# Kernel tuning notes

Measured on AMD Instinct MI355X. Metric: run time of the kernel, lower is better.

Reference implementation:

```python
import jax, jax.numpy as jnp
import numpy as np

NPOINT = 1024
NSAMPLE = 32
RADIUS = 0.2


def index_points2(points, idx):
    # points: (B,N,D), idx: (B,S) -> (B,S,D)
    return jnp.take_along_axis(points, idx[..., None], axis=1)


def index_points3(points, idx):
    # points: (B,N,D), idx: (B,S,K) -> (B,S,K,D)
    B, S, K = idx.shape
    flat = jnp.take_along_axis(points, idx.reshape(B, S * K)[..., None], axis=1)
    return flat.reshape(B, S, K, points.shape[-1])


def farthest_point_sampling(xyz, npoint):
    # xyz: (B,N,3) -> (B,npoint) int32 indices. First point deterministic (index 0).
    B, N, _ = xyz.shape
    first = jnp.zeros((B,), jnp.int32)
    chosen = jnp.zeros((B, npoint), jnp.int32).at[:, 0].set(first)
    first_xyz = index_points2(xyz, first[:, None])[:, 0, :]
    dist_min = jnp.sum((xyz - first_xyz[:, None, :]) ** 2, axis=-1)  # (B,N)

    def body(i, carry):
        chosen, dist_min = carry
        far = jnp.argmax(dist_min, axis=-1).astype(jnp.int32)  # (B,)
        far_xyz = index_points2(xyz, far[:, None])[:, 0, :]
        d = jnp.sum((xyz - far_xyz[:, None, :]) ** 2, axis=-1)
        return chosen.at[:, i].set(far), jnp.minimum(dist_min, d)

    chosen, _ = jax.lax.fori_loop(1, npoint, body, (chosen, dist_min))
    return chosen


def query_ball_point(radius, nsample, xyz, new_xyz):
    # (B,S,N) squared distances; out-of-ball -> inf; take nsample nearest (stable argsort).
    dist = jnp.sum((new_xyz[:, :, None, :] - xyz[:, None, :, :]) ** 2, axis=-1)
    dist_m = jnp.where(dist <= radius ** 2, dist, jnp.inf)
    return jnp.argsort(dist_m, axis=-1)[:, :, :nsample]


def mlp2(x, Wa, ba, Wb, bb, act2):
    h = jax.nn.relu(x @ Wa + ba)
    return act2(h @ Wb + bb)


def reference(xyz, features, W1, b1, W2, b2, W3, b3, W4, b4):
    fps_idx = farthest_point_sampling(xyz, NPOINT)          # (B,S)
    new_xyz = index_points2(xyz, fps_idx)                   # (B,S,3)
    group_idx = query_ball_point(RADIUS, NSAMPLE, xyz, new_xyz)  # (B,S,K)
    grouped_xyz = index_points3(xyz, group_idx)             # (B,S,K,3)
    grouped_xyz_norm = grouped_xyz - new_xyz[:, :, None, :]
    grouped_feats = index_points3(features, group_idx)      # (B,S,K,C)
    f_in = jnp.concatenate([grouped_xyz_norm, grouped_feats], axis=-1)
    f_prime = mlp2(f_in, W1, b1, W2, b2, jax.nn.relu)       # (B,S,K,H)
    f_mean = jnp.mean(f_prime, axis=2, keepdims=True)
    w_in = jnp.concatenate([grouped_xyz_norm, f_prime - f_mean], axis=-1)
    alpha = mlp2(w_in, W3, b3, W4, b4, jax.nn.sigmoid)      # (B,S,K,H)
    f_out = jnp.sum(alpha * f_prime, axis=2)                # (B,S,H)
    return new_xyz, f_out


def setup_inputs() -> dict:
    key = jax.random.key(0)
    ks = jax.random.split(key, 8)
    B, N, C, H = 16, 4096, 64, 128
    xyz = jax.random.uniform(ks[0], (B, N, 3), dtype=jnp.float32)
    features = jax.random.normal(ks[1], (B, N, C), dtype=jnp.float32)
    s = 0.1
    return {
        "xyz": xyz,
        "features": features,
        "W1": jax.random.normal(ks[2], (3 + C, H), dtype=jnp.float32) * s,
        "b1": jnp.zeros((H,), jnp.float32),
        "W2": jax.random.normal(ks[3], (H, H), dtype=jnp.float32) * s,
        "b2": jnp.zeros((H,), jnp.float32),
        "W3": jax.random.normal(ks[4], (3 + H, H), dtype=jnp.float32) * s,
        "b3": jnp.zeros((H,), jnp.float32),
        "W4": jax.random.normal(ks[5], (H, H), dtype=jnp.float32) * s,
        "b4": jnp.zeros((H,), jnp.float32),
    }
```

## Files before the change

kernel.cpp:

```cpp
#include <hip/hip_runtime.h>

typedef unsigned short u16;
typedef unsigned int   u32;
typedef unsigned long long u64;
typedef short s8v __attribute__((ext_vector_type(8)));
typedef float f4v __attribute__((ext_vector_type(4)));
typedef float f2v __attribute__((ext_vector_type(2)));

#define STRIDE 168
#define CAP 256
#define OFF_G1 0
#define OFF_G2 12288
#define OFF_G3 28672
#define OFF_G4 49152

__device__ __forceinline__ float bf2f(u16 u){ return __uint_as_float(((u32)u)<<16); }
__device__ __forceinline__ u16 f2bf(float f){
  u32 u = __float_as_uint(f);
  return (u16)((u + 0x7FFFu + ((u>>16)&1u)) >> 16);
}
__device__ __forceinline__ float sqd(float ax,float ay,float az,float bx,float by,float bz){
  float dx=ax-bx, dy=ay-by, dz=az-bz;
  return __fadd_rn(__fadd_rn(__fmul_rn(dx,dx),__fmul_rn(dy,dy)),__fmul_rn(dz,dz));
}

#define WMAX_STEP(v, CTRL) { \
  u32 _t = (u32)__builtin_amdgcn_update_dpp(0, (int)(v), CTRL, 0xf, 0xf, false); \
  (v) = (v) > _t ? (v) : _t; }
#define QMAX64(k, CTRL) { \
  u32 _lo=(u32)(k), _hi=(u32)((k)>>32); \
  u32 _plo=(u32)__builtin_amdgcn_update_dpp(0,(int)_lo,CTRL,0xf,0xf,true); \
  u32 _phi=(u32)__builtin_amdgcn_update_dpp(0,(int)_hi,CTRL,0xf,0xf,true); \
  u64 _o=((u64)_phi<<32)|_plo; (k) = (k)>_o ? (k) : _o; }

__global__ __launch_bounds__(256) void fps_kernel(const float* __restrict__ xyz,
                                                  float* __restrict__ newxyz){
  __shared__ __align__(16) float S[4096*3];
  __shared__ __align__(16) float R[1024*3];
  __shared__ u64 red[2][4];
  const int b = blockIdx.x, tid = threadIdx.x;
  const int lane = tid & 63, wv = tid >> 6;
  const float* xb = xyz + (size_t)b*4096*3;
  #pragma unroll
  for(int j=0;j<12;j++) ((float4*)S)[j*256+tid] = ((const float4*)xb)[j*256+tid];
  __syncthreads();
  f2v X[8],Y[8],Z[8],DM[8];
  const float x0=S[0], y0=S[1], z0=S[2];
  {
    #pragma clang fp contract(off)
    const f2v fx2={x0,x0}, fy2={y0,y0}, fz2={z0,z0};
    #pragma unroll
    for(int k2=0;k2<8;k2++){
      int p0 = tid*16 + 2*k2;
      X[k2] = (f2v){S[p0*3],   S[p0*3+3]};
      Y[k2] = (f2v){S[p0*3+1], S[p0*3+4]};
      Z[k2] = (f2v){S[p0*3+2], S[p0*3+5]};
      f2v dx=X[k2]-fx2, dy=Y[k2]-fy2, dz=Z[k2]-fz2;
      DM[k2] = (dx*dx + dy*dy) + dz*dz;
    }
  }
  if(tid==0){ R[0]=x0; R[1]=y0; R[2]=z0; }
  for(int i=1;i<1024;i++){
    f2v a = __builtin_elementwise_max(__builtin_elementwise_max(DM[0],DM[1]),
                                      __builtin_elementwise_max(DM[2],DM[3]));
    f2v c = __builtin_elementwise_max(__builtin_elementwise_max(DM[4],DM[5]),
                                      __builtin_elementwise_max(DM[6],DM[7]));
    f2v mm = __builtin_elementwise_max(a,c);
    float vm = fmaxf(mm[0], mm[1]);
    u32 m16 = 0;
    #pragma unroll
    for(int j=0;j<16;j++) m16 |= (DM[j>>1][j&1]==vm) ? (1u<<j) : 0u;
    int jm = __ffs(m16)-1;
    u32 w = __float_as_uint(vm);
    WMAX_STEP(w, 0x111); WMAX_STEP(w, 0x112); WMAX_STEP(w, 0x114);
    WMAX_STEP(w, 0x118); WMAX_STEP(w, 0x142); WMAX_STEP(w, 0x143);
    u32 wm = (u32)__builtin_amdgcn_readlane((int)w, 63);
    u64 msk = __ballot(__float_as_uint(vm) == wm);
    int ldr = __ffsll((unsigned long long)msk) - 1;
    int pj  = __builtin_amdgcn_readlane(jm, ldr);
    int p   = (wv*64 + ldr)*16 + pj;
    if(lane==0) red[i&1][wv] = ((u64)wm<<32) | (u32)(~(u32)p);
    __syncthreads();
    u64 k = red[i&1][lane&3];
    QMAX64(k, 0xB1); QMAX64(k, 0x4E);
    int far = (int)(~(u32)k) & 4095;
    float fx=S[far*3], fy=S[far*3+1], fz=S[far*3+2];
    if(tid==0){ R[i*3]=fx; R[i*3+1]=fy; R[i*3+2]=fz; }
    {
      #pragma clang fp contract(off)
      const f2v fx2={fx,fx}, fy2={fy,fy}, fz2={fz,fz};
      #pragma unroll
      for(int k2c=0;k2c<8;k2c++){
        f2v dx=X[k2c]-fx2, dy=Y[k2c]-fy2, dz=Z[k2c]-fz2;
        f2v s = (dx*dx + dy*dy) + dz*dz;
        DM[k2c] = __builtin_elementwise_min(DM[k2c], s);
      }
    }
  }
  __syncthreads();
  float* nb = newxyz + (size_t)b*3072;
  #pragma unroll
  for(int j=0;j<3;j++) ((float4*)nb)[j*256+tid] = ((const float4*)R)[j*256+tid];
}

__global__ __launch_bounds__(256) void swz_kernel(const float* __restrict__ W1,const float* __restrict__ W2,
                                                  const float* __restrict__ W3,const float* __restrict__ W4,
                                                  u16* __restrict__ wsw){
  int T = blockIdx.x*256 + threadIdx.x;
  const float* W; int rel, base, kind;
  if(T < 1536){ rel=T;      base=OFF_G1; W=W1; kind=0; }
  else if(T < 3584){ rel=T-1536; base=OFF_G2; W=W2; kind=1; }
  else if(T < 6144){ rel=T-3584; base=OFF_G3; W=W3; kind=0; }
  else         { rel=T-6144; base=OFF_G4; W=W4; kind=1; }
  int chunk=rel>>6, lane=rel&63, c=chunk>>3, t=chunk&7, quad=lane>>4, l15=lane&15;
  u16 v[8];
  #pragma unroll
  for(int j=0;j<8;j++){
    int kp = c*32 + quad*8 + j, n = t*16 + l15;
    int src = (kind==0) ? (kp<3 ? kp : (kp>=32 ? kp-29 : -1)) : kp;
    v[j] = (src<0) ? (u16)0 : f2bf(W[src*128 + n]);
  }
  int4 o;
  o.x=(int)((u32)v[0]|((u32)v[1]<<16)); o.y=(int)((u32)v[2]|((u32)v[3]<<16));
  o.z=(int)((u32)v[4]|((u32)v[5]<<16)); o.w=(int)((u32)v[6]|((u32)v[7]<<16));
  *(int4*)&wsw[base + rel*8] = o;
}

__device__ __forceinline__ void zero_C(f4v C[2][8]){
  #pragma unroll
  for(int mt=0;mt<2;mt++)
    #pragma unroll
    for(int t=0;t<8;t++) C[mt][t] = (f4v){0.f,0.f,0.f,0.f};
}
__device__ __forceinline__ void load_bias(const float* bsrc,int l15,float bb[8]){
  #pragma unroll
  for(int t=0;t<8;t++) bb[t]=bsrc[t*16+l15];
}
template<int KC>
__device__ __forceinline__ void run_gemm(const u16* A, const u16* BW,
                                         int lane,int l15,int quad, f4v C[2][8]){
  s8v af[2][KC];
  #pragma unroll
  for(int mt=0;mt<2;mt++)
    #pragma unroll
    for(int c=0;c<KC;c++)
      af[mt][c] = *(const s8v*)&A[(mt*16+l15)*STRIDE + c*32 + quad*8];
  #pragma unroll
  for(int t=0;t<8;t++){
    #pragma unroll
    for(int c=0;c<KC;c++){
      s8v bw = *(const s8v*)&BW[((c*8+t)*64 + lane)*8];
      C[0][t] = __builtin_amdgcn_mfma_f32_16x16x32_bf16(af[0][c],bw,C[0][t],0,0,0);
      C[1][t] = __builtin_amdgcn_mfma_f32_16x16x32_bf16(af[1][c],bw,C[1][t],0,0,0);
    }
  }
}
__device__ __forceinline__ void store_act(u16* A,int l15,int quad,f4v C[2][8],const float bb[8]){
  #pragma unroll
  for(int mt=0;mt<2;mt++)
    #pragma unroll
    for(int t=0;t<8;t++)
      #pragma unroll
      for(int r=0;r<4;r++){
        float v = fmaxf(C[mt][t][r]+bb[t], 0.f);
        A[(mt*16+quad*4+r)*STRIDE + t*16 + l15] = f2bf(v);
      }
}
__device__ __forceinline__ void write_xyz_chunk0(u16* A,int lane,float xn,float yn,float zn){
  if(lane<32){
    u16* row=&A[lane*STRIDE];
    row[0]=f2bf(xn); row[1]=f2bf(yn); row[2]=f2bf(zn); row[3]=0;
    #pragma unroll
    for(int q=0;q<7;q++) *(u64*)&row[4+q*4] = 0ull;
  }
}

__global__ __launch_bounds__(256,3) void mlp_kernel(const float* __restrict__ xyz,
    const float* __restrict__ feats, const u16* __restrict__ wsw,
    const float* __restrict__ b1,const float* __restrict__ b2,const float* __restrict__ b3,const float* __restrict__ b4,
    const float* __restrict__ newxyz, float* __restrict__ fout){
  __shared__ __align__(16) u16 Abuf[4][32*STRIDE];
  __shared__ u64 Bcand[4][CAP];
  __shared__ int selbuf[4][32];
  const int tid=threadIdx.x, wv=tid>>6, lane=tid&63, quad=lane>>4, l15=lane&15;
  const int widx = blockIdx.x*4 + wv, b = widx>>10;
  u16* A = Abuf[wv];
  const float* xb = xyz + (size_t)b*4096*3;
  const float cx=newxyz[widx*3], cy=newxyz[widx*3+1], cz=newxyz[widx*3+2];

  {
    u64* Bc = Bcand[wv];
    int* sel = selbuf[wv];
    const u64 lt = (1ull<<lane)-1ull;
    int base=0;
    for(int kk=0;kk<64;kk++){
      int p = kk*64 + lane;
      float d = sqd(cx,cy,cz, xb[p*3],xb[p*3+1],xb[p*3+2]);
      bool in = (d <= 0.04f);
      u64 m = __ballot(in);
      if(in){ int pos = base + __popcll(m&lt); if(pos<CAP) Bc[pos] = ((u64)__float_as_uint(d)<<32)|(u32)p; }
      base += __popcll(m);
    }
    int cnt = base>CAP ? CAP : base;
    if(cnt > 32){
      for(int c=lane; c<cnt; c+=64){
        u64 key = Bc[c]; int r=0;
        for(int t2=0;t2<cnt;t2++) r += (Bc[t2] < key) ? 1 : 0;
        if(r < 32) sel[r] = (int)(u32)key;
      }
    } else {
      for(int c=lane; c<cnt; c+=64) sel[c] = (int)(u32)Bc[c];
      int need = 32 - cnt, b2 = 0;
      for(int kk=0; kk<64 && b2<need; kk++){
        int p = kk*64 + lane;
        float d = sqd(cx,cy,cz, xb[p*3],xb[p*3+1],xb[p*3+2]);
        bool o = !(d <= 0.04f);
        u64 m = __ballot(o);
        if(o){ int pos = b2 + __popcll(m&lt); if(pos<need) sel[cnt+pos] = p; }
        b2 += __popcll(m);
      }
    }
  }
  const int* sel = selbuf[wv];
  const int gi_f = sel[lane>>1] & 4095;
  const int gi_x = sel[lane & 31] & 4095;

  {
    int r2=lane>>1, h=lane&1;
    const float* fs = feats + ((size_t)b*4096 + gi_f)*64 + h*32;
    u16* fd = &A[r2*STRIDE + 32 + h*32];
    #pragma unroll
    for(int j=0;j<8;j++){
      float4 v4 = ((const float4*)fs)[j];
      u64 pk4 = (u64)f2bf(v4.x) | ((u64)f2bf(v4.y)<<16)
              | ((u64)f2bf(v4.z)<<32) | ((u64)f2bf(v4.w)<<48);
      *(u64*)&fd[j*4] = pk4;
    }
  }
  float xn=0.f,yn=0.f,zn=0.f;
  if(lane<32){
    const float* xp = xb + (size_t)gi_x*3;
    xn = xp[0]-cx; yn = xp[1]-cy; zn = xp[2]-cz;
  }
  write_xyz_chunk0(A,lane,xn,yn,zn);
  __syncthreads();

  f4v C[2][8]; float bb[8];
  zero_C(C); load_bias(b1,l15,bb);
  run_gemm<3>(A, wsw+OFF_G1, lane,l15,quad, C);
  store_act(A,l15,quad,C,bb);
  __syncthreads();
  zero_C(C); load_bias(b2,l15,bb);
  run_gemm<4>(A, wsw+OFF_G2, lane,l15,quad, C);
  float fp[2][8][4]; float mean[8];
  #pragma unroll
  for(int t=0;t<8;t++){
    float s=0.f;
    #pragma unroll
    for(int mt=0;mt<2;mt++)
      #pragma unroll
      for(int r=0;r<4;r++){
        float v = fmaxf(C[mt][t][r]+bb[t], 0.f);
        fp[mt][t][r]=v; s+=v;
      }
    s += __shfl_xor(s,16); s += __shfl_xor(s,32);
    mean[t] = s*0.03125f;
  }
  #pragma unroll
  for(int mt=0;mt<2;mt++)
    #pragma unroll
    for(int t=0;t<8;t++)
      #pragma unroll
      for(int r=0;r<4;r++)
        A[(mt*16+quad*4+r)*STRIDE + 32 + t*16 + l15] = f2bf(fp[mt][t][r]-mean[t]);
  write_xyz_chunk0(A,lane,xn,yn,zn);
  __syncthreads();
  zero_C(C); load_bias(b3,l15,bb);
  run_gemm<5>(A, wsw+OFF_G3, lane,l15,quad, C);
  store_act(A,l15,quad,C,bb);
  __syncthreads();
  zero_C(C); load_bias(b4,l15,bb);
  run_gemm<4>(A, wsw+OFF_G4, lane,l15,quad, C);
  float* fo = fout + (size_t)widx*128;
  #pragma unroll
  for(int t=0;t<8;t++){
    float part=0.f;
    #pragma unroll
    for(int mt=0;mt<2;mt++)
      #pragma unroll
      for(int r=0;r<4;r++){
        float pre = C[mt][t][r]+bb[t];
        float a = 1.f/(1.f+__expf(-pre));
        part += a*fp[mt][t][r];
      }
    part += __shfl_xor(part,16); part += __shfl_xor(part,32);
    if(quad==0) fo[t*16+l15] = part;
  }
}

extern "C" void kernel_launch(void* const* d_in, const int* in_sizes, int n_in,
                              void* d_out, int out_size, void* d_ws, size_t ws_size,
                              hipStream_t stream){
  (void)in_sizes; (void)n_in; (void)out_size; (void)ws_size;
  const float* xyz   = (const float*)d_in[0];
  const float* feats = (const float*)d_in[1];
  const float* W1 = (const float*)d_in[2]; const float* b1 = (const float*)d_in[3];
  const float* W2 = (const float*)d_in[4]; const float* b2 = (const float*)d_in[5];
  const float* W3 = (const float*)d_in[6]; const float* b3 = (const float*)d_in[7];
  const float* W4 = (const float*)d_in[8]; const float* b4 = (const float*)d_in[9];
  float* out = (float*)d_out;
  float* newxyz = out;
  float* fout   = out + 16*1024*3;
  u16* wsw = (u16*)d_ws;

  hipLaunchKernelGGL(swz_kernel, dim3(32),   dim3(256), 0, stream, W1,W2,W3,W4, wsw);
  hipLaunchKernelGGL(fps_kernel, dim3(16),   dim3(256), 0, stream, xyz, newxyz);
  hipLaunchKernelGGL(mlp_kernel, dim3(4096), dim3(256), 0, stream,
                     xyz, feats, wsw, b1,b2,b3,b4, newxyz, fout);
}
```

Measured before the change: 1.010 ms.

## Run FPS in a single wave and split ball query into its own kernel

FPS now runs one 64-lane wave per batch with 64 points per lane held in registers. It uses a tree argmax with indices, so the cross-wave LDS reduction and the __syncthreads in each of the 1023 iterations go away. Ball query moves out of the MLP kernel into a separate kernel that writes the selected indices into the fout buffer as scratch, and its rank-sort reads two keys at a time. The MLP kernel then only reads those indices, which frees its LDS and may raise occupancy. The cost is an extra launch, a global round-trip for the indices, and much higher register pressure in FPS, which runs on only 16 waves.

```diff
diff --git a/kernel.cpp b/kernel.cpp
--- a/kernel.cpp
+++ b/kernel.cpp
@@ -6,6 +6,8 @@
 typedef short s8v __attribute__((ext_vector_type(8)));
 typedef float f4v __attribute__((ext_vector_type(4)));
 typedef float f2v __attribute__((ext_vector_type(2)));
+typedef int   i2v __attribute__((ext_vector_type(2)));
+typedef unsigned long long ull2 __attribute__((ext_vector_type(2)));
 
 #define STRIDE 168
 #define CAP 256
@@ -27,50 +29,46 @@
 #define WMAX_STEP(v, CTRL) { \
   u32 _t = (u32)__builtin_amdgcn_update_dpp(0, (int)(v), CTRL, 0xf, 0xf, false); \
   (v) = (v) > _t ? (v) : _t; }
-#define QMAX64(k, CTRL) { \
-  u32 _lo=(u32)(k), _hi=(u32)((k)>>32); \
-  u32 _plo=(u32)__builtin_amdgcn_update_dpp(0,(int)_lo,CTRL,0xf,0xf,true); \
-  u32 _phi=(u32)__builtin_amdgcn_update_dpp(0,(int)_hi,CTRL,0xf,0xf,true); \
-  u64 _o=((u64)_phi<<32)|_plo; (k) = (k)>_o ? (k) : _o; }
-
-__global__ __launch_bounds__(256) void fps_kernel(const float* __restrict__ xyz,
-                                                  float* __restrict__ newxyz){
-  __shared__ __align__(16) float S[4096*3];
+
+__global__ __launch_bounds__(64,1) void fps_kernel(const float* __restrict__ xyz,
+                                                   float* __restrict__ newxyz){
+  __shared__ __align__(16) float SX[64][66], SY[64][66], SZ[64][66];
   __shared__ __align__(16) float R[1024*3];
-  __shared__ u64 red[2][4];
-  const int b = blockIdx.x, tid = threadIdx.x;
-  const int lane = tid & 63, wv = tid >> 6;
+  const int b = blockIdx.x, lane = threadIdx.x;
   const float* xb = xyz + (size_t)b*4096*3;
-  #pragma unroll
-  for(int j=0;j<12;j++) ((float4*)S)[j*256+tid] = ((const float4*)xb)[j*256+tid];
-  __syncthreads();
-  f2v X[8],Y[8],Z[8],DM[8];
-  const float x0=S[0], y0=S[1], z0=S[2];
+  for(int j=0;j<64;j++){
+    int p = j*64 + lane;
+    SX[j][lane] = xb[p*3]; SY[j][lane] = xb[p*3+1]; SZ[j][lane] = xb[p*3+2];
+  }
+  f2v X[32],Y[32],Z[32],DM[32];
+  const float x0=SX[0][0], y0=SY[0][0], z0=SZ[0][0];
   {
     #pragma clang fp contract(off)
     const f2v fx2={x0,x0}, fy2={y0,y0}, fz2={z0,z0};
     #pragma unroll
-    for(int k2=0;k2<8;k2++){
-      int p0 = tid*16 + 2*k2;
-      X[k2] = (f2v){S[p0*3],   S[p0*3+3]};
-      Y[k2] = (f2v){S[p0*3+1], S[p0*3+4]};
-      Z[k2] = (f2v){S[p0*3+2], S[p0*3+5]};
-      f2v dx=X[k2]-fx2, dy=Y[k2]-fy2, dz=Z[k2]-fz2;
-      DM[k2] = (dx*dx + dy*dy) + dz*dz;
-    }
-  }
-  if(tid==0){ R[0]=x0; R[1]=y0; R[2]=z0; }
+    for(int k=0;k<32;k++){
+      X[k] = (f2v){SX[lane][k], SX[lane][k+32]};
+      Y[k] = (f2v){SY[lane][k], SY[lane][k+32]};
+      Z[k] = (f2v){SZ[lane][k], SZ[lane][k+32]};
+      f2v dx=X[k]-fx2, dy=Y[k]-fy2, dz=Z[k]-fz2;
+      DM[k] = (dx*dx + dy*dy) + dz*dz;
+    }
+  }
+  if(lane==0){ R[0]=x0; R[1]=y0; R[2]=z0; }
   for(int i=1;i<1024;i++){
-    f2v a = __builtin_elementwise_max(__builtin_elementwise_max(DM[0],DM[1]),
-                                      __builtin_elementwise_max(DM[2],DM[3]));
-    f2v c = __builtin_elementwise_max(__builtin_elementwise_max(DM[4],DM[5]),
-                                      __builtin_elementwise_max(DM[6],DM[7]));
-    f2v mm = __builtin_elementwise_max(a,c);
-    float vm = fmaxf(mm[0], mm[1]);
-    u32 m16 = 0;
-    #pragma unroll
-    for(int j=0;j<16;j++) m16 |= (DM[j>>1][j&1]==vm) ? (1u<<j) : 0u;
-    int jm = __ffs(m16)-1;
+    f2v v[32]; i2v ix[32];
+    #pragma unroll
+    for(int k=0;k<32;k++){ v[k]=DM[k]; ix[k]=(i2v){k, k+32}; }
+    #pragma unroll
+    for(int n=32;n>1;n>>=1)
+      #pragma unroll
+      for(int k=0;k<(n>>1);k++){
+        i2v c = v[2*k+1] > v[2*k];
+        v[k]  = c ? v[2*k+1] : v[2*k];
+        ix[k] = c ? ix[2*k+1] : ix[2*k];
+      }
+    float vm; int jm;
+    { bool g = v[0][1] > v[0][0]; vm = g ? v[0][1] : v[0][0]; jm = g ? ix[0][1] : ix[0][0]; }
     u32 w = __float_as_uint(vm);
     WMAX_STEP(w, 0x111); WMAX_STEP(w, 0x112); WMAX_STEP(w, 0x114);
     WMAX_STEP(w, 0x118); WMAX_STEP(w, 0x142); WMAX_STEP(w, 0x143);
@@ -78,29 +76,69 @@
     u64 msk = __ballot(__float_as_uint(vm) == wm);
     int ldr = __ffsll((unsigned long long)msk) - 1;
     int pj  = __builtin_amdgcn_readlane(jm, ldr);
-    int p   = (wv*64 + ldr)*16 + pj;
-    if(lane==0) red[i&1][wv] = ((u64)wm<<32) | (u32)(~(u32)p);
-    __syncthreads();
-    u64 k = red[i&1][lane&3];
-    QMAX64(k, 0xB1); QMAX64(k, 0x4E);
-    int far = (int)(~(u32)k) & 4095;
-    float fx=S[far*3], fy=S[far*3+1], fz=S[far*3+2];
-    if(tid==0){ R[i*3]=fx; R[i*3+1]=fy; R[i*3+2]=fz; }
+    float fx=SX[ldr][pj], fy=SY[ldr][pj], fz=SZ[ldr][pj];
+    if(lane==0){ R[i*3]=fx; R[i*3+1]=fy; R[i*3+2]=fz; }
     {
       #pragma clang fp contract(off)
       const f2v fx2={fx,fx}, fy2={fy,fy}, fz2={fz,fz};
       #pragma unroll
-      for(int k2c=0;k2c<8;k2c++){
-        f2v dx=X[k2c]-fx2, dy=Y[k2c]-fy2, dz=Z[k2c]-fz2;
+      for(int k=0;k<32;k++){
+        f2v dx=X[k]-fx2, dy=Y[k]-fy2, dz=Z[k]-fz2;
         f2v s = (dx*dx + dy*dy) + dz*dz;
-        DM[k2c] = __builtin_elementwise_min(DM[k2c], s);
-      }
-    }
-  }
-  __syncthreads();
+        DM[k] = __builtin_elementwise_min(DM[k], s);
+      }
+    }
+  }
   float* nb = newxyz + (size_t)b*3072;
   #pragma unroll
-  for(int j=0;j<3;j++) ((float4*)nb)[j*256+tid] = ((const float4*)R)[j*256+tid];
+  for(int j=0;j<12;j++) ((float4*)nb)[j*64+lane] = ((const float4*)R)[j*64+lane];
+}
+
+__global__ __launch_bounds__(256) void ballq_kernel(const float* __restrict__ xyz,
+                                                    const float* __restrict__ newxyz,
+                                                    int* __restrict__ selg){
+  __shared__ u64 Bc4[4][CAP+2];
+  const int tid=threadIdx.x, wv=tid>>6, lane=tid&63;
+  const int widx = blockIdx.x*4 + wv, b = widx>>10;
+  const float* xb = xyz + (size_t)b*4096*3;
+  const float cx=newxyz[widx*3], cy=newxyz[widx*3+1], cz=newxyz[widx*3+2];
+  u64* Bc = Bc4[wv];
+  int* selp = selg + (size_t)widx*128;
+  const u64 lt = (1ull<<lane)-1ull;
+  int base=0;
+  for(int kk=0;kk<64;kk++){
+    int p = kk*64 + lane;
+    float d = sqd(cx,cy,cz, xb[p*3],xb[p*3+1],xb[p*3+2]);
+    bool in = (d <= 0.04f);
+    u64 m = __ballot(in);
+    if(in){ int pos = base + __popcll(m&lt); if(pos<CAP) Bc[pos] = ((u64)__float_as_uint(d)<<32)|(u32)p; }
+    base += __popcll(m);
+  }
+  int cnt = base>CAP ? CAP : base;
+  if(cnt > 32){
+    if(lane==0){ Bc[cnt]=~0ull; Bc[cnt+1]=~0ull; }
+    int cnt2 = (cnt+1)&~1;
+    for(int c=lane; c<cnt; c+=64){
+      u64 key = Bc[c]; int r=0;
+      for(int t2=0;t2<cnt2;t2+=2){
+        ull2 k2 = *(const ull2*)&Bc[t2];
+        r += (k2[0] < key) ? 1 : 0;
+        r += (k2[1] < key) ? 1 : 0;
+      }
+      if(r < 32) selp[r] = (int)(u32)key;
+    }
+  } else {
+    for(int c=lane; c<cnt; c+=64) selp[c] = (int)(u32)Bc[c];
+    int need = 32 - cnt, b2 = 0;
+    for(int kk=0; kk<64 && b2<need; kk++){
+      int p = kk*64 + lane;
+      float d = sqd(cx,cy,cz, xb[p*3],xb[p*3+1],xb[p*3+2]);
+      bool o = !(d <= 0.04f);
+      u64 m = __ballot(o);
+      if(o){ int pos = b2 + __popcll(m&lt); if(pos<need) selp[cnt+pos] = p; }
+      b2 += __popcll(m);
+    }
+  }
 }
 
 __global__ __launch_bounds__(256) void swz_kernel(const float* __restrict__ W1,const float* __restrict__ W2,
@@ -180,50 +218,14 @@
     const float* __restrict__ b1,const float* __restrict__ b2,const float* __restrict__ b3,const float* __restrict__ b4,
     const float* __restrict__ newxyz, float* __restrict__ fout){
   __shared__ __align__(16) u16 Abuf[4][32*STRIDE];
-  __shared__ u64 Bcand[4][CAP];
-  __shared__ int selbuf[4][32];
   const int tid=threadIdx.x, wv=tid>>6, lane=tid&63, quad=lane>>4, l15=lane&15;
   const int widx = blockIdx.x*4 + wv, b = widx>>10;
   u16* A = Abuf[wv];
   const float* xb = xyz + (size_t)b*4096*3;
   const float cx=newxyz[widx*3], cy=newxyz[widx*3+1], cz=newxyz[widx*3+2];
-
-  {
-    u64* Bc = Bcand[wv];
-    int* sel = selbuf[wv];
-    const u64 lt = (1ull<<lane)-1ull;
-    int base=0;
-    for(int kk=0;kk<64;kk++){
-      int p = kk*64 + lane;
-      float d = sqd(cx,cy,cz, xb[p*3],xb[p*3+1],xb[p*3+2]);
-      bool in = (d <= 0.04f);
-      u64 m = __ballot(in);
-      if(in){ int pos = base + __popcll(m&lt); if(pos<CAP) Bc[pos] = ((u64)__float_as_uint(d)<<32)|(u32)p; }
-      base += __popcll(m);
-    }
-    int cnt = base>CAP ? CAP : base;
-    if(cnt > 32){
-      for(int c=lane; c<cnt; c+=64){
-        u64 key = Bc[c]; int r=0;
-        for(int t2=0;t2<cnt;t2++) r += (Bc[t2] < key) ? 1 : 0;
-        if(r < 32) sel[r] = (int)(u32)key;
-      }
-    } else {
-      for(int c=lane; c<cnt; c+=64) sel[c] = (int)(u32)Bc[c];
-      int need = 32 - cnt, b2 = 0;
-      for(int kk=0; kk<64 && b2<need; kk++){
-        int p = kk*64 + lane;
-        float d = sqd(cx,cy,cz, xb[p*3],xb[p*3+1],xb[p*3+2]);
-        bool o = !(d <= 0.04f);
-        u64 m = __ballot(o);
-        if(o){ int pos = b2 + __popcll(m&lt); if(pos<need) sel[cnt+pos] = p; }
-        b2 += __popcll(m);
-      }
-    }
-  }
-  const int* sel = selbuf[wv];
-  const int gi_f = sel[lane>>1] & 4095;
-  const int gi_x = sel[lane & 31] & 4095;
+  const int* selp = (const int*)(fout + (size_t)widx*128);
+  const int gi_f = selp[lane>>1] & 4095;
+  const int gi_x = selp[lane & 31] & 4095;
 
   {
     int r2=lane>>1, h=lane&1;
@@ -313,8 +315,9 @@
   float* fout   = out + 16*1024*3;
   u16* wsw = (u16*)d_ws;
 
-  hipLaunchKernelGGL(swz_kernel, dim3(32),   dim3(256), 0, stream, W1,W2,W3,W4, wsw);
-  hipLaunchKernelGGL(fps_kernel, dim3(16),   dim3(256), 0, stream, xyz, newxyz);
-  hipLaunchKernelGGL(mlp_kernel, dim3(4096), dim3(256), 0, stream,
+  hipLaunchKernelGGL(swz_kernel,   dim3(32),   dim3(256), 0, stream, W1,W2,W3,W4, wsw);
+  hipLaunchKernelGGL(fps_kernel,   dim3(16),   dim3(64),  0, stream, xyz, newxyz);
+  hipLaunchKernelGGL(ballq_kernel, dim3(4096), dim3(256), 0, stream, xyz, newxyz, (int*)fout);
+  hipLaunchKernelGGL(mlp_kernel,   dim3(4096), dim3(256), 0, stream,
                      xyz, feats, wsw, b1,b2,b3,b4, newxyz, fout);
 }
```

Result: slower. 1.751 ms (+73.3%).
